# Optimization experiments

Measured on AMD Instinct MI355X. Metric: run time of the kernel, lower is better.

## Reference

```python
import jax, jax.numpy as jnp
import numpy as np

B = 64
N_SNPS = 500000
N_GENES = 20000
N_NODES = 600000
N_FILTERS = 8
EPS = 1e-5  # torch BatchNorm1d default


def setup_inputs() -> dict:
    key = jax.random.key(0)
    ks = jax.random.split(key, 14)
    snp = jax.random.normal(ks[0], (B, N_SNPS), dtype=jnp.float32)
    snp_ids = jax.random.randint(ks[1], (N_NODES,), 0, N_SNPS, dtype=jnp.int32)
    node_gene = jax.random.randint(ks[2], (N_NODES,), 0, N_GENES, dtype=jnp.int32)
    # learned params
    filters = jax.random.normal(ks[3], (N_FILTERS, N_SNPS), dtype=jnp.float32) * 0.001
    W1 = jax.random.normal(ks[4], (N_GENES, 1024), dtype=jnp.float32) * 0.02
    b1 = jnp.zeros((1024,), jnp.float32)
    g1 = 1.0 + 0.02 * jax.random.normal(ks[5], (1024,), dtype=jnp.float32)
    beta1 = jnp.zeros((1024,), jnp.float32)
    W2 = jax.random.normal(ks[6], (1024, 256), dtype=jnp.float32) * 0.02
    b2 = jnp.zeros((256,), jnp.float32)
    g2 = 1.0 + 0.02 * jax.random.normal(ks[7], (256,), dtype=jnp.float32)
    beta2 = jnp.zeros((256,), jnp.float32)
    W3 = jax.random.normal(ks[8], (256, 1), dtype=jnp.float32) * 0.02
    b3 = jnp.zeros((1,), jnp.float32)
    return {"snp": snp, "snp_ids": snp_ids, "node_gene": node_gene,
            "filters": filters, "W1": W1, "b1": b1, "g1": g1, "beta1": beta1,
            "W2": W2, "b2": b2, "g2": g2, "beta2": beta2, "W3": W3, "b3": b3}


def _batchnorm(x, gamma, beta):
    # training-mode batch statistics over the batch axis (biased var)
    m = jnp.mean(x, axis=0)
    v = jnp.var(x, axis=0)
    return gamma * (x - m) * jax.lax.rsqrt(v + EPS) + beta


def reference(snp, snp_ids, node_gene, filters, W1, b1, g1, beta1,
              W2, b2, g2, beta2, W3, b3):
    # Original: snp_h[b,n,f] = snp[b,n]*filters[f,n]; per-sample gather by snp_ids,
    # DGL sum-readout per gene, then mean over filter channel. Since readout-sum
    # and channel-mean are linear, fuse: per-SNP weight = mean_f filters[f,:].
    w = jnp.mean(filters, axis=0)                      # [n_snps]
    node = snp[:, snp_ids] * w[snp_ids][None, :]       # [B, n_nodes]
    gene = jnp.zeros((snp.shape[0], N_GENES), snp.dtype)
    gene = gene.at[:, node_gene].add(node)             # batched segment-sum -> [B, n_genes]
    # predictor MLP (dropout = identity in eval; BN uses batch stats)
    h = jax.nn.relu(_batchnorm(gene @ W1 + b1, g1, beta1))
    h = jax.nn.relu(_batchnorm(h @ W2 + b2, g2, beta2))
    preds = h @ W3 + b3                                # [B, 1]
    return preds, filters
```

## Files before the change

kernel.cpp:

```cpp
#include <hip/hip_runtime.h>

#define NS 500000
#define NG 20000
#define NN 600000
#define NF 8
#define EPS_ 1e-5f

__global__ __launch_bounds__(256) void k_w_copy(const float* __restrict__ filters,
                                                float* __restrict__ w,
                                                float* __restrict__ out_f) {
  int i = blockIdx.x * 256 + threadIdx.x;
  const int n4 = NS / 4;
  if (i >= n4) return;
  const float4* f4 = (const float4*)filters;
  float4* o4 = (float4*)out_f;
  float sx = 0.f, sy = 0.f, sz = 0.f, sw = 0.f;
#pragma unroll
  for (int f = 0; f < NF; f++) {
    float4 v = f4[(size_t)f * n4 + i];
    o4[(size_t)f * n4 + i] = v;
    sx += v.x; sy += v.y; sz += v.z; sw += v.w;
  }
  float4 r;
  r.x = sx * 0.125f; r.y = sy * 0.125f; r.z = sz * 0.125f; r.w = sw * 0.125f;
  ((float4*)w)[i] = r;
}

__global__ __launch_bounds__(256) void k_hist_mark(const int* __restrict__ snp_ids,
                                                   const int* __restrict__ node_gene,
                                                   int* __restrict__ cnt,
                                                   unsigned char* __restrict__ used) {
  int j = blockIdx.x * 256 + threadIdx.x;
  if (j < NN) {
    used[snp_ids[j]] = 1;
    atomicAdd(&cnt[node_gene[j]], 1);
  }
}

__global__ __launch_bounds__(1024) void k_scan(const int* __restrict__ cnt,
                                               int* __restrict__ offs,
                                               int* __restrict__ cursor) {
  __shared__ int part[1024];
  int t = threadIdx.x;
  int base = t * 20;
  int s = 0;
  for (int i = 0; i < 20; i++) {
    int g = base + i;
    if (g < NG) s += cnt[g];
  }
  part[t] = s;
  __syncthreads();
  for (int d = 1; d < 1024; d <<= 1) {
    int v = 0;
    if (t >= d) v = part[t - d];
    __syncthreads();
    part[t] += v;
    __syncthreads();
  }
  int run = part[t] - s;
  for (int i = 0; i < 20; i++) {
    int g = base + i;
    if (g < NG) {
      offs[g] = run;
      cursor[g] = run;
      run += cnt[g];
    }
  }
  if (t == 1023) offs[NG] = part[1023];
}

__global__ __launch_bounds__(256) void k_sortnodes(const int* __restrict__ snp_ids,
                                                   const int* __restrict__ node_gene,
                                                   int* __restrict__ cursor,
                                                   int* __restrict__ sorted_sid) {
  int j = blockIdx.x * 256 + threadIdx.x;
  if (j >= NN) return;
  int g = node_gene[j];
  int pos = atomicAdd(&cursor[g], 1);
  sorted_sid[pos] = snp_ids[j];
}

__global__ __launch_bounds__(256) void k_transpose(const float* __restrict__ snp,
                                                   const float* __restrict__ w,
                                                   const unsigned char* __restrict__ used,
                                                   float* __restrict__ snpT) {
  __shared__ float tile[64 * 64];
  int t = threadIdx.x;
  int s0 = blockIdx.x * 64;

  int f = t & 15;
  int r = (t >> 4) & 3;
  int wq = t >> 6;
  float4 w4 = make_float4(0.f, 0.f, 0.f, 0.f);
  if (s0 + 4 * f + 4 <= NS) w4 = *(const float4*)(w + s0 + 4 * f);
#pragma unroll
  for (int i = 0; i < 4; i++) {
    int b = wq * 16 + i * 4 + r;
    float4 v = make_float4(0.f, 0.f, 0.f, 0.f);
    if (s0 + 4 * f + 4 <= NS) v = *(const float4*)(snp + (size_t)b * NS + s0 + 4 * f);
    v.x *= w4.x; v.y *= w4.y; v.z *= w4.z; v.w *= w4.w;
    ((float4*)tile)[b * 16 + (f ^ (b & 15))] = v;
  }
  __syncthreads();

  int b = t & 63;
  int sq = t >> 6;
  int ubase = s0 + sq * 16;
  unsigned u32s[4];
  if (ubase + 16 <= NS) {
    uint4 ub = *(const uint4*)(used + ubase);
    u32s[0] = ub.x; u32s[1] = ub.y; u32s[2] = ub.z; u32s[3] = ub.w;
  } else {
#pragma unroll
    for (int i = 0; i < 4; i++) {
      unsigned v = 0;
#pragma unroll
      for (int k = 0; k < 4; k++) {
        int s = ubase + 4 * i + k;
        if (s < NS && used[s]) v |= (1u << (8 * k));
      }
      u32s[i] = v;
    }
  }
#pragma unroll
  for (int i = 0; i < 4; i++) {
    int s4 = sq * 4 + i;
    float4 x = ((const float4*)tile)[b * 16 + (s4 ^ (b & 15))];
    int sb = s0 + 4 * s4;
    float xv[4] = {x.x, x.y, x.z, x.w};
#pragma unroll
    for (int k = 0; k < 4; k++) {
      int s = sb + k;
      bool u = ((u32s[i] >> (8 * k)) & 0xFFu) != 0;
      if (s < NS && u) snpT[(size_t)s * 64 + b] = xv[k];
    }
  }
}

__global__ __launch_bounds__(256) void k_accum_T(const float* __restrict__ snpT,
                                                 const int* __restrict__ offs,
                                                 const int* __restrict__ sorted_sid,
                                                 float* __restrict__ geneT) {
  int wave = (blockIdx.x * 256 + threadIdx.x) >> 6;
  int lane = threadIdx.x & 63;
  if (wave >= NG) return;
  int beg = offs[wave], end = offs[wave + 1];
  float a0 = 0.f, a1 = 0.f, a2 = 0.f, a3 = 0.f;
  int n = beg;
  for (; n + 8 <= end; n += 8) {
    int i0 = sorted_sid[n + 0];
    int i1 = sorted_sid[n + 1];
    int i2 = sorted_sid[n + 2];
    int i3 = sorted_sid[n + 3];
    int i4 = sorted_sid[n + 4];
    int i5 = sorted_sid[n + 5];
    int i6 = sorted_sid[n + 6];
    int i7 = sorted_sid[n + 7];
    float v0 = snpT[(size_t)i0 * 64 + lane];
    float v1 = snpT[(size_t)i1 * 64 + lane];
    float v2 = snpT[(size_t)i2 * 64 + lane];
    float v3 = snpT[(size_t)i3 * 64 + lane];
    float v4 = snpT[(size_t)i4 * 64 + lane];
    float v5 = snpT[(size_t)i5 * 64 + lane];
    float v6 = snpT[(size_t)i6 * 64 + lane];
    float v7 = snpT[(size_t)i7 * 64 + lane];
    a0 += v0; a1 += v1; a2 += v2; a3 += v3;
    a0 += v4; a1 += v5; a2 += v6; a3 += v7;
  }
  for (; n + 4 <= end; n += 4) {
    int i0 = sorted_sid[n + 0];
    int i1 = sorted_sid[n + 1];
    int i2 = sorted_sid[n + 2];
    int i3 = sorted_sid[n + 3];
    a0 += snpT[(size_t)i0 * 64 + lane];
    a1 += snpT[(size_t)i1 * 64 + lane];
    a2 += snpT[(size_t)i2 * 64 + lane];
    a3 += snpT[(size_t)i3 * 64 + lane];
  }
  for (; n < end; n++) a0 += snpT[(size_t)sorted_sid[n] * 64 + lane];
  geneT[(size_t)wave * 64 + lane] = (a0 + a1) + (a2 + a3);
}

template <int NCOLS, int KPSMAX>
__global__ __launch_bounds__(256) void k_gemm_stream(const float* __restrict__ XT,
                                                     const float* __restrict__ Wm,
                                                     float* __restrict__ partial,
                                                     int KTOT, int kPerSlice) {
  __shared__ float xs[KPSMAX * 64];
  int tid = threadIdx.x;
  int lane = tid & 63;
  int wv = tid >> 6;
  int c0 = blockIdx.x * 256 + lane * 4;
  int b0 = wv * 16;
  int kBeg = blockIdx.y * kPerSlice;
  int kEnd = KTOT < kBeg + kPerSlice ? KTOT : kBeg + kPerSlice;
  int kc = kEnd - kBeg;

  {
    const float4* src = (const float4*)(XT + (size_t)kBeg * 64);
    float4* dst = (float4*)xs;
    for (int i = tid; i < kc * 16; i += 256) dst[i] = src[i];
  }
  __syncthreads();

  float acc[4][16];
#pragma unroll
  for (int i = 0; i < 4; i++)
#pragma unroll
    for (int j = 0; j < 16; j++) acc[i][j] = 0.f;

#pragma unroll 2
  for (int kk = 0; kk < kc; kk++) {
    float4 wr = *(const float4*)(Wm + (size_t)(kBeg + kk) * NCOLS + c0);
    const float4* xp = (const float4*)(xs + kk * 64 + b0);
    float4 g0 = xp[0], g1 = xp[1], g2 = xp[2], g3 = xp[3];
    float gg[16];
    gg[0] = g0.x; gg[1] = g0.y; gg[2] = g0.z; gg[3] = g0.w;
    gg[4] = g1.x; gg[5] = g1.y; gg[6] = g1.z; gg[7] = g1.w;
    gg[8] = g2.x; gg[9] = g2.y; gg[10] = g2.z; gg[11] = g2.w;
    gg[12] = g3.x; gg[13] = g3.y; gg[14] = g3.z; gg[15] = g3.w;
#pragma unroll
    for (int j = 0; j < 16; j++) {
      acc[0][j] = fmaf(wr.x, gg[j], acc[0][j]);
      acc[1][j] = fmaf(wr.y, gg[j], acc[1][j]);
      acc[2][j] = fmaf(wr.z, gg[j], acc[2][j]);
      acc[3][j] = fmaf(wr.w, gg[j], acc[3][j]);
    }
  }

  float* pb = partial + (size_t)blockIdx.y * NCOLS * 64;
#pragma unroll
  for (int i = 0; i < 4; i++) {
    float4* dst = (float4*)(pb + (size_t)(c0 + i) * 64 + b0);
#pragma unroll
    for (int q = 0; q < 4; q++) {
      float4 v;
      v.x = acc[i][q * 4 + 0]; v.y = acc[i][q * 4 + 1];
      v.z = acc[i][q * 4 + 2]; v.w = acc[i][q * 4 + 3];
      dst[q] = v;
    }
  }
}

__global__ __launch_bounds__(256) void k_reduce_bn(const float* __restrict__ partial,
                                                   int S, int ncols,
                                                   const float* __restrict__ gamma,
                                                   const float* __restrict__ beta,
                                                   float* __restrict__ outT) {
  int n = blockIdx.x * 4 + (threadIdx.x >> 6);
  int b = threadIdx.x & 63;
  size_t stride = (size_t)ncols * 64;
  const float* p = partial + (size_t)n * 64 + b;
  float x0 = 0.f, x1 = 0.f, x2 = 0.f, x3 = 0.f;
  int s = 0;
  for (; s + 4 <= S; s += 4) {
    x0 += p[(size_t)(s + 0) * stride];
    x1 += p[(size_t)(s + 1) * stride];
    x2 += p[(size_t)(s + 2) * stride];
    x3 += p[(size_t)(s + 3) * stride];
  }
  for (; s < S; s++) x0 += p[(size_t)s * stride];
  float x = (x0 + x1) + (x2 + x3);
  float s1 = x, s2 = x * x;
#pragma unroll
  for (int d = 32; d > 0; d >>= 1) {
    s1 += __shfl_xor(s1, d, 64);
    s2 += __shfl_xor(s2, d, 64);
  }
  float m = s1 * (1.f / 64.f);
  float v = s2 * (1.f / 64.f) - m * m;
  float y = gamma[n] * (x - m) * rsqrtf(v + EPS_) + beta[n];
  outT[(size_t)n * 64 + b] = fmaxf(y, 0.f);
}

__global__ __launch_bounds__(64) void k_head(const float* __restrict__ h2T,
                                             const float* __restrict__ W3,
                                             const float* __restrict__ b3,
                                             float* __restrict__ out) {
  int b = threadIdx.x;
  float acc = 0.f;
  for (int k = 0; k < 256; k++) acc = fmaf(h2T[(size_t)k * 64 + b], W3[k], acc);
  out[b] = acc + b3[0];
}

static constexpr int S1 = 128;
static constexpr int S2 = 128;
static constexpr size_t N_W = NS;
static constexpr size_t N_SNPT = (size_t)NS * 64;
static constexpr size_t N_GENET = (size_t)NG * 64;
static constexpr size_t N_P1 = (size_t)S1 * 1024 * 64;
static constexpr size_t N_P2 = (size_t)S2 * 256 * 64;

extern "C" void kernel_launch(void* const* d_in, const int* in_sizes, int n_in,
                              void* d_out, int out_size, void* d_ws, size_t ws_size,
                              hipStream_t stream) {
  const float* snp       = (const float*)d_in[0];
  const int*   snp_ids   = (const int*)d_in[1];
  const int*   node_gene = (const int*)d_in[2];
  const float* filters   = (const float*)d_in[3];
  const float* W1        = (const float*)d_in[4];
  const float* g1        = (const float*)d_in[6];
  const float* beta1     = (const float*)d_in[7];
  const float* W2        = (const float*)d_in[8];
  const float* g2        = (const float*)d_in[10];
  const float* beta2     = (const float*)d_in[11];
  const float* W3        = (const float*)d_in[12];
  const float* b3        = (const float*)d_in[13];
  float* out = (float*)d_out;
  float* ws  = (float*)d_ws;

  float* w      = ws;
  float* snpT   = ws + N_W;
  float* p1     = snpT;
  float* p2     = p1 + N_P1;
  float* geneT  = snpT + N_SNPT;
  float* h1T    = geneT + N_GENET;
  float* h2T    = h1T + 65536;
  int* cnt      = (int*)(h2T + 16384);
  int* offs     = cnt + NG;
  int* cursor   = offs + 20064;
  int* sorted   = cursor + NG;
  unsigned char* used = (unsigned char*)(sorted + NN);

  hipMemsetAsync(cnt, 0, NG * sizeof(int), stream);
  hipMemsetAsync(used, 0, NS, stream);

  k_w_copy<<<(NS / 4 + 255) / 256, 256, 0, stream>>>(filters, w, out + 64);

  k_hist_mark<<<(NN + 255) / 256, 256, 0, stream>>>(snp_ids, node_gene, cnt, used);
  k_scan<<<1, 1024, 0, stream>>>(cnt, offs, cursor);
  k_sortnodes<<<(NN + 255) / 256, 256, 0, stream>>>(snp_ids, node_gene, cursor, sorted);

  k_transpose<<<(NS + 63) / 64, 256, 0, stream>>>(snp, w, used, snpT);
  k_accum_T<<<(NG * 64) / 256, 256, 0, stream>>>(snpT, offs, sorted, geneT);

  int kps1 = (NG + S1 - 1) / S1;
  k_gemm_stream<1024, 157><<<dim3(4, S1), 256, 0, stream>>>(geneT, W1, p1, NG, kps1);
  k_reduce_bn<<<1024 / 4, 256, 0, stream>>>(p1, S1, 1024, g1, beta1, h1T);

  int kps2 = 1024 / S2;
  k_gemm_stream<256, 8><<<dim3(1, S2), 256, 0, stream>>>(h1T, W2, p2, 1024, kps2);
  k_reduce_bn<<<256 / 4, 256, 0, stream>>>(p2, S2, 256, g2, beta2, h2T);

  k_head<<<1, 64, 0, stream>>>(h2T, W3, b3, out);
}
```

Before: 509.7 us.

## Prefetch W rows in GEMM, relayout partials per column, and split K finer

The streaming GEMM now loads weight rows two iterations ahead into registers to hide global load latency. Partial sums are stored with the slice index adjacent to the column, so the reduce+BN kernel reads contiguous memory, and the reduction is unrolled by eight. The first GEMM's K is split into 250 slices of 80 rows instead of 128 slices, launching more blocks to fill the GPU. The cost is more partial-sum traffic and a larger workspace.

```diff
diff --git a/kernel.cpp b/kernel.cpp
--- a/kernel.cpp
+++ b/kernel.cpp
@@ -192,6 +192,7 @@
   int wv = tid >> 6;
   int c0 = blockIdx.x * 256 + lane * 4;
   int b0 = wv * 16;
+  int nslice = gridDim.y;
   int kBeg = blockIdx.y * kPerSlice;
   int kEnd = KTOT < kBeg + kPerSlice ? KTOT : kBeg + kPerSlice;
   int kc = kEnd - kBeg;
@@ -209,9 +210,16 @@
 #pragma unroll
     for (int j = 0; j < 16; j++) acc[i][j] = 0.f;
 
+  const float* wp = Wm + (size_t)kBeg * NCOLS + c0;
+  float4 w0 = make_float4(0.f, 0.f, 0.f, 0.f);
+  float4 w1 = make_float4(0.f, 0.f, 0.f, 0.f);
+  if (kc > 0) w0 = *(const float4*)(wp);
+  if (kc > 1) w1 = *(const float4*)(wp + NCOLS);
+
+  int kk = 0;
 #pragma unroll 2
-  for (int kk = 0; kk < kc; kk++) {
-    float4 wr = *(const float4*)(Wm + (size_t)(kBeg + kk) * NCOLS + c0);
+  for (; kk + 2 < kc; kk++) {
+    float4 wn = *(const float4*)(wp + (size_t)(kk + 2) * NCOLS);
     const float4* xp = (const float4*)(xs + kk * 64 + b0);
     float4 g0 = xp[0], g1 = xp[1], g2 = xp[2], g3 = xp[3];
     float gg[16];
@@ -221,17 +229,34 @@
     gg[12] = g3.x; gg[13] = g3.y; gg[14] = g3.z; gg[15] = g3.w;
 #pragma unroll
     for (int j = 0; j < 16; j++) {
-      acc[0][j] = fmaf(wr.x, gg[j], acc[0][j]);
-      acc[1][j] = fmaf(wr.y, gg[j], acc[1][j]);
-      acc[2][j] = fmaf(wr.z, gg[j], acc[2][j]);
-      acc[3][j] = fmaf(wr.w, gg[j], acc[3][j]);
-    }
-  }
-
-  float* pb = partial + (size_t)blockIdx.y * NCOLS * 64;
+      acc[0][j] = fmaf(w0.x, gg[j], acc[0][j]);
+      acc[1][j] = fmaf(w0.y, gg[j], acc[1][j]);
+      acc[2][j] = fmaf(w0.z, gg[j], acc[2][j]);
+      acc[3][j] = fmaf(w0.w, gg[j], acc[3][j]);
+    }
+    w0 = w1; w1 = wn;
+  }
+  for (; kk < kc; kk++) {
+    const float4* xp = (const float4*)(xs + kk * 64 + b0);
+    float4 g0 = xp[0], g1 = xp[1], g2 = xp[2], g3 = xp[3];
+    float gg[16];
+    gg[0] = g0.x; gg[1] = g0.y; gg[2] = g0.z; gg[3] = g0.w;
+    gg[4] = g1.x; gg[5] = g1.y; gg[6] = g1.z; gg[7] = g1.w;
+    gg[8] = g2.x; gg[9] = g2.y; gg[10] = g2.z; gg[11] = g2.w;
+    gg[12] = g3.x; gg[13] = g3.y; gg[14] = g3.z; gg[15] = g3.w;
+#pragma unroll
+    for (int j = 0; j < 16; j++) {
+      acc[0][j] = fmaf(w0.x, gg[j], acc[0][j]);
+      acc[1][j] = fmaf(w0.y, gg[j], acc[1][j]);
+      acc[2][j] = fmaf(w0.z, gg[j], acc[2][j]);
+      acc[3][j] = fmaf(w0.w, gg[j], acc[3][j]);
+    }
+    w0 = w1;
+  }
+
 #pragma unroll
   for (int i = 0; i < 4; i++) {
-    float4* dst = (float4*)(pb + (size_t)(c0 + i) * 64 + b0);
+    float4* dst = (float4*)(partial + ((size_t)(c0 + i) * nslice + blockIdx.y) * 64 + b0);
 #pragma unroll
     for (int q = 0; q < 4; q++) {
       float4 v;
@@ -243,24 +268,28 @@
 }
 
 __global__ __launch_bounds__(256) void k_reduce_bn(const float* __restrict__ partial,
-                                                   int S, int ncols,
+                                                   int S,
                                                    const float* __restrict__ gamma,
                                                    const float* __restrict__ beta,
                                                    float* __restrict__ outT) {
   int n = blockIdx.x * 4 + (threadIdx.x >> 6);
   int b = threadIdx.x & 63;
-  size_t stride = (size_t)ncols * 64;
-  const float* p = partial + (size_t)n * 64 + b;
+  const float* p = partial + (size_t)n * S * 64 + b;
   float x0 = 0.f, x1 = 0.f, x2 = 0.f, x3 = 0.f;
+  float x4 = 0.f, x5 = 0.f, x6 = 0.f, x7 = 0.f;
   int s = 0;
-  for (; s + 4 <= S; s += 4) {
-    x0 += p[(size_t)(s + 0) * stride];
-    x1 += p[(size_t)(s + 1) * stride];
-    x2 += p[(size_t)(s + 2) * stride];
-    x3 += p[(size_t)(s + 3) * stride];
-  }
-  for (; s < S; s++) x0 += p[(size_t)s * stride];
-  float x = (x0 + x1) + (x2 + x3);
+  for (; s + 8 <= S; s += 8) {
+    x0 += p[(s + 0) * 64];
+    x1 += p[(s + 1) * 64];
+    x2 += p[(s + 2) * 64];
+    x3 += p[(s + 3) * 64];
+    x4 += p[(s + 4) * 64];
+    x5 += p[(s + 5) * 64];
+    x6 += p[(s + 6) * 64];
+    x7 += p[(s + 7) * 64];
+  }
+  for (; s < S; s++) x0 += p[s * 64];
+  float x = ((x0 + x1) + (x2 + x3)) + ((x4 + x5) + (x6 + x7));
   float s1 = x, s2 = x * x;
 #pragma unroll
   for (int d = 32; d > 0; d >>= 1) {
@@ -283,7 +312,7 @@
   out[b] = acc + b3[0];
 }
 
-static constexpr int S1 = 128;
+static constexpr int S1 = 250;
 static constexpr int S2 = 128;
 static constexpr size_t N_W = NS;
 static constexpr size_t N_SNPT = (size_t)NS * 64;
@@ -334,13 +363,11 @@
   k_transpose<<<(NS + 63) / 64, 256, 0, stream>>>(snp, w, used, snpT);
   k_accum_T<<<(NG * 64) / 256, 256, 0, stream>>>(snpT, offs, sorted, geneT);
 
-  int kps1 = (NG + S1 - 1) / S1;
-  k_gemm_stream<1024, 157><<<dim3(4, S1), 256, 0, stream>>>(geneT, W1, p1, NG, kps1);
-  k_reduce_bn<<<1024 / 4, 256, 0, stream>>>(p1, S1, 1024, g1, beta1, h1T);
-
-  int kps2 = 1024 / S2;
-  k_gemm_stream<256, 8><<<dim3(1, S2), 256, 0, stream>>>(h1T, W2, p2, 1024, kps2);
-  k_reduce_bn<<<256 / 4, 256, 0, stream>>>(p2, S2, 256, g2, beta2, h2T);
+  k_gemm_stream<1024, 80><<<dim3(4, S1), 256, 0, stream>>>(geneT, W1, p1, NG, 80);
+  k_reduce_bn<<<1024 / 4, 256, 0, stream>>>(p1, S1, g1, beta1, h1T);
+
+  k_gemm_stream<256, 8><<<dim3(1, S2), 256, 0, stream>>>(h1T, W2, p2, 1024, 8);
+  k_reduce_bn<<<256 / 4, 256, 0, stream>>>(p2, S2, g2, beta2, h2T);
 
   k_head<<<1, 64, 0, stream>>>(h2T, W3, b3, out);
 }
```

Result: faster. 490.0 us (-3.9%).
